# Performance work log

Measured on AMD Instinct MI355X. Metric: run time of the kernel, lower is better.

Reference implementation:

```python
import jax, jax.numpy as jnp
import numpy as np

DN = ('NCH', 'OIH', 'NCH')  # conv dimension numbers: [batch, channel, length]

def setup_inputs() -> dict:
    key = jax.random.key(0)
    ks = jax.random.split(key, 8)
    B, S, L, D, F, V = 16, 64, 128, 512, 256, 30000
    return {
        'text': jax.random.randint(ks[0], (B, S, L), 0, V),
        'embed': jax.random.normal(ks[1], (V, D), dtype=jnp.float32),
        'w3': jax.random.normal(ks[2], (F, D, 3), dtype=jnp.float32) * 0.05,
        'b3': jax.random.normal(ks[3], (F,), dtype=jnp.float32) * 0.05,
        'w4': jax.random.normal(ks[4], (F, D, 4), dtype=jnp.float32) * 0.05,
        'b4': jax.random.normal(ks[5], (F,), dtype=jnp.float32) * 0.05,
        'w5': jax.random.normal(ks[6], (F, D, 5), dtype=jnp.float32) * 0.05,
        'b5': jax.random.normal(ks[7], (F,), dtype=jnp.float32) * 0.05,
    }

def reference(text, embed, w3, b3, w4, b4, w5, b5):
    B, S, L = text.shape
    # Embed tokens, flatten episodes x utterances into one batch, channels-first.
    x = embed[text]                                   # [B, S, L, D]
    x = x.reshape(B * S, L, -1).transpose(0, 2, 1)    # [BS, D, L]
    outs = []
    for w, b in ((w3, b3), (w4, b4), (w5, b5)):
        y = jax.lax.conv_general_dilated(x, w, (1,), 'VALID', dimension_numbers=DN)
        # max-over-time pooling (valid conv -> length L-K+1)
        outs.append(jnp.max(y + b[None, :, None], axis=2))  # [BS, F]
    out = jax.nn.relu(jnp.concatenate(outs, axis=1))  # [BS, 3F]
    return out.reshape(B, S, -1)
```

## Files before the change

### kernel.cpp

```cpp
#include <hip/hip_runtime.h>
#include <hip/hip_bf16.h>


typedef __bf16 bf16x8 __attribute__((ext_vector_type(8)));
typedef float f32x16 __attribute__((ext_vector_type(16)));
typedef float f32x4v __attribute__((ext_vector_type(4)));

#define ROWS 132
#define ROWB 512
#define BUF_BYTES (ROWS * ROWB)
#define RED_OFF (2 * BUF_BYTES)
#define LDS_TOTAL (RED_OFF + 2048)

__global__ void pack_w_kernel(const float* __restrict__ w3,
                              const float* __restrict__ w4,
                              const float* __restrict__ w5,
                              __bf16* __restrict__ wq) {
    const int t    = blockIdx.x * 256 + threadIdx.x;
    const int g    = t >> 6;
    const int lane = t & 63;
    int rel, Kw; const float* w;
    if (g < 768)       { rel = g;        Kw = 3; w = w3; }
    else if (g < 1792) { rel = g - 768;  Kw = 4; w = w4; }
    else               { rel = g - 1792; Kw = 5; w = w5; }
    const int k16 = rel >> 3;
    const int n32 = rel & 7;
    const int f   = n32 * 32 + (lane & 31);
    const int tap = k16 >> 5;
    const int d0  = (k16 & 31) * 16 + (lane >> 5) * 8;
    const float* src = w + ((size_t)f * 512 + d0) * Kw + tap;
    bf16x8 o;
#pragma unroll
    for (int j = 0; j < 8; ++j) o[j] = (__bf16)src[j * Kw];
    *(bf16x8*)(wq + (size_t)t * 8) = o;
}

__global__ __launch_bounds__(1024, 4) void conv_gemm_kernel(
        const int* __restrict__ text,
        const float* __restrict__ embed,
        const __bf16* __restrict__ wq,
        const float* __restrict__ b3,
        const float* __restrict__ b4,
        const float* __restrict__ b5,
        float* __restrict__ out) {
    extern __shared__ char lds[];
    float* const red = (float*)(lds + RED_OFF);

    const int tid  = threadIdx.x;
    const int lane = tid & 63;
    const int wave = tid >> 6;
    const int wm   = wave & 1;
    const int wn   = wave >> 1;
    const int l31  = lane & 31;
    const int lh   = lane >> 5;
    const int sr   = tid >> 5;
    const int sc   = tid & 31;

    const int bsbase = blockIdx.x * 4;

    const int arow = wm * 64 + l31;
    const int tx0  = lh ^ (arow & 31);
    const int A00  = arow * 512;

    const __bf16* const bpL = wq + (size_t)wn * 512 + (size_t)lane * 8;

    f32x4v G[4];
    auto issuePair = [&](int nbs, int h, int p0) {
#pragma unroll
        for (int p = 0; p < 2; ++p) {
            const int r = (p0 + p) * 32 + sr;
            const int tok = text[nbs * 128 + r];
            const f32x4v* src = (const f32x4v*)
                (embed + (size_t)tok * 512 + h * 256 + sc * 8);
            G[p * 2]     = __builtin_nontemporal_load(src);
            G[p * 2 + 1] = __builtin_nontemporal_load(src + 1);
        }
    };
    auto writePair = [&](char* bufp, int p0) {
#pragma unroll
        for (int p = 0; p < 2; ++p) {
            const int r = (p0 + p) * 32 + sr;
            const f32x4v v0 = G[p * 2], v1 = G[p * 2 + 1];
            bf16x8 o;
            o[0] = (__bf16)v0.x; o[1] = (__bf16)v0.y;
            o[2] = (__bf16)v0.z; o[3] = (__bf16)v0.w;
            o[4] = (__bf16)v1.x; o[5] = (__bf16)v1.y;
            o[6] = (__bf16)v1.z; o[7] = (__bf16)v1.w;
            *(bf16x8*)(bufp + r * ROWB + ((sc ^ (r & 31)) << 4)) = o;
        }
    };

    f32x16 acc[2];
    bf16x8 Br[4];
    bf16x8 A[4][2];

    issuePair(bsbase, 0, 0); writePair(lds, 0);
    issuePair(bsbase, 0, 2); writePair(lds, 2);
    issuePair(bsbase, 1, 0); writePair(lds + BUF_BYTES, 0);
    issuePair(bsbase, 1, 2); writePair(lds + BUF_BYTES, 2);
    if (tid < 128) {
        const int r = 128 + sr;
        const int off = r * ROWB + ((sc ^ (r & 31)) << 4);
        bf16x8 z = {};
        *(bf16x8*)(lds + off) = z;
        *(bf16x8*)(lds + BUF_BYTES + off) = z;
    }
#pragma unroll
    for (int k = 0; k < 4; ++k)
        Br[k] = *(const bf16x8*)(bpL + (size_t)k * 4096);
    __syncthreads();

#pragma unroll 1
    for (int i = 0; i < 4; ++i) {
        const int bs  = bsbase + i;
        const int nbs = bs + 1;
        const bool stg = (i < 3);
#pragma unroll 1
        for (int c = 0; c < 3; ++c) {
            const int KW = 3 + c;
            const size_t cb  = (c == 0) ? 0 : (c == 1) ? 393216 : 917504;
            const size_t cbn = (c == 0) ? 393216 : (c == 1) ? 917504 : 0;
            const __bf16* bpc = bpL + cb;
            const __bf16* bpn = bpL + cbn;
            const bool lastc = stg && (c == 2);

#pragma unroll
            for (int r = 0; r < 16; ++r) { acc[0][r] = 0.f; acc[1][r] = 0.f; }

            if (lastc) issuePair(nbs, 0, 0);

            A[0][0] = *(const bf16x8*)(lds + A00 + (tx0 << 4));
            A[0][1] = *(const bf16x8*)(lds + A00 + (tx0 << 4) + 16384);
            A[1][0] = *(const bf16x8*)(lds + A00 + ((2 ^ tx0) << 4));
            A[1][1] = *(const bf16x8*)(lds + A00 + ((2 ^ tx0) << 4) + 16384);

#pragma unroll 1
            for (int tap = 0; tap < KW; ++tap) {
                const int row = arow + tap;
                const int tx  = lh ^ (row & 31);
                const int rb  = row * 512;
                const bool last = (tap == KW - 1);
                const int r2  = row + 1;
                const int tx2 = lh ^ (r2 & 31);
                const int rb2 = r2 * 512;
#pragma unroll
                for (int dh = 0; dh < 2; ++dh) {
                    const int bo = dh ? BUF_BYTES : 0;
                    const int s0 = tap * 32 + dh * 16;
                    const __bf16* q0 = bpc + (size_t)(s0 + 4) * 4096;
                    const __bf16* q1 = (dh == 1 && tap == KW - 1)
                                           ? bpn : (q0 + 12 * 4096);
#pragma unroll
                    for (int d = 0; d < 16; ++d) {
                        const int s = dh * 16 + d;
                        const int u = s + 2;
                        int na;
                        if (u < 16)
                            na = rb + (((2 * u) ^ tx) << 4);
                        else if (u < 32)
                            na = BUF_BYTES + rb + (((2 * (u - 16)) ^ tx) << 4);
                        else if (!last)
                            na = rb2 + (((2 * (u - 32)) ^ tx2) << 4);
                        else
                            na = rb + (tx << 4);
                        const int cs = s & 3, ps = u & 3;
                        __builtin_amdgcn_s_setprio(1);
                        acc[0] = __builtin_amdgcn_mfma_f32_32x32x16_bf16(
                            A[cs][0], Br[cs], acc[0], 0, 0, 0);
                        acc[1] = __builtin_amdgcn_mfma_f32_32x32x16_bf16(
                            A[cs][1], Br[cs], acc[1], 0, 0, 0);
                        __builtin_amdgcn_s_setprio(0);
                        A[ps][0] = *(const bf16x8*)(lds + na);
                        A[ps][1] = *(const bf16x8*)(lds + na + 16384);
                        Br[cs] = (d < 12)
                            ? *(const bf16x8*)(q0 + (size_t)d * 4096)
                            : *(const bf16x8*)(q1 + (size_t)(d - 12) * 4096);
                    }
                }
            }

            const int Tv = 126 - c;
            float cmax = -3.0e38f;
#pragma unroll
            for (int mt = 0; mt < 2; ++mt)
#pragma unroll
                for (int r = 0; r < 16; ++r) {
                    const int t = wm * 64 + mt * 32
                                + (r & 3) + 8 * (r >> 2) + 4 * lh;
                    if (t < Tv) cmax = fmaxf(cmax, acc[mt][r]);
                }
            cmax = fmaxf(cmax, __shfl_xor(cmax, 32, 64));

            __syncthreads();
            if (lane < 32) red[wm * 256 + wn * 32 + l31] = cmax;
            if (lastc) {
                writePair(lds, 0);
                issuePair(nbs, 0, 2); writePair(lds, 2);
                issuePair(nbs, 1, 0); writePair(lds + BUF_BYTES, 0);
                issuePair(nbs, 1, 2); writePair(lds + BUF_BYTES, 2);
            }
            __syncthreads();
            if (tid < 256) {
                const float* bias = (c == 0) ? b3 : (c == 1) ? b4 : b5;
                const float vv = fmaxf(red[tid], red[256 + tid]) + bias[tid];
                __builtin_nontemporal_store(fmaxf(vv, 0.f),
                    &out[(size_t)bs * 768 + c * 256 + tid]);
            }
        }
    }
}

extern "C" void kernel_launch(void* const* d_in, const int* in_sizes, int n_in,
                              void* d_out, int out_size, void* d_ws, size_t ws_size,
                              hipStream_t stream) {
    const int*   text  = (const int*)d_in[0];
    const float* embed = (const float*)d_in[1];
    const float* w3    = (const float*)d_in[2];
    const float* b3    = (const float*)d_in[3];
    const float* w4    = (const float*)d_in[4];
    const float* b4    = (const float*)d_in[5];
    const float* w5    = (const float*)d_in[6];
    const float* b5    = (const float*)d_in[7];
    float* out = (float*)d_out;

    __bf16* wq = (__bf16*)d_ws;

    (void)hipFuncSetAttribute((const void*)conv_gemm_kernel,
                              hipFuncAttributeMaxDynamicSharedMemorySize,
                              LDS_TOTAL);

    pack_w_kernel<<<768, 256, 0, stream>>>(w3, w4, w5, wq);
    conv_gemm_kernel<<<256, 1024, LDS_TOTAL, stream>>>(text, embed, wq,
                                                       b3, b4, b5, out);
}
```

Before: 493.9 us.

## Halve block to 512 threads with 2x2 MFMA tiles per wave

Reduces the conv GEMM block from 16 to 8 waves, so each wave now computes two N-tiles (64 filters) instead of one. A-fragments read from LDS are reused across two B fragments, which halves LDS A traffic per MFMA and doubles accumulator registers. Embedding staging is reworked to 16 rows per pass with four row-groups. Fewer waves per CU cut latency hiding, and register pressure rises from the larger accumulators and B buffers.

```diff
diff --git a/kernel.cpp b/kernel.cpp
--- a/kernel.cpp
+++ b/kernel.cpp
@@ -35,7 +35,7 @@
     *(bf16x8*)(wq + (size_t)t * 8) = o;
 }
 
-__global__ __launch_bounds__(1024, 4) void conv_gemm_kernel(
+__global__ __launch_bounds__(512, 2) void conv_gemm_kernel(
         const int* __restrict__ text,
         const float* __restrict__ embed,
         const __bf16* __restrict__ wq,
@@ -62,13 +62,13 @@
     const int tx0  = lh ^ (arow & 31);
     const int A00  = arow * 512;
 
-    const __bf16* const bpL = wq + (size_t)wn * 512 + (size_t)lane * 8;
-
-    f32x4v G[4];
-    auto issuePair = [&](int nbs, int h, int p0) {
-#pragma unroll
-        for (int p = 0; p < 2; ++p) {
-            const int r = (p0 + p) * 32 + sr;
+    const __bf16* const bpL = wq + (size_t)wn * 1024 + (size_t)lane * 8;
+
+    f32x4v G[8];
+    auto issueQuad = [&](int nbs, int h, int p0) {
+#pragma unroll
+        for (int p = 0; p < 4; ++p) {
+            const int r = (p0 + p) * 16 + sr;
             const int tok = text[nbs * 128 + r];
             const f32x4v* src = (const f32x4v*)
                 (embed + (size_t)tok * 512 + h * 256 + sc * 8);
@@ -76,10 +76,10 @@
             G[p * 2 + 1] = __builtin_nontemporal_load(src + 1);
         }
     };
-    auto writePair = [&](char* bufp, int p0) {
-#pragma unroll
-        for (int p = 0; p < 2; ++p) {
-            const int r = (p0 + p) * 32 + sr;
+    auto writeQuad = [&](char* bufp, int p0) {
+#pragma unroll
+        for (int p = 0; p < 4; ++p) {
+            const int r = (p0 + p) * 16 + sr;
             const f32x4v v0 = G[p * 2], v1 = G[p * 2 + 1];
             bf16x8 o;
             o[0] = (__bf16)v0.x; o[1] = (__bf16)v0.y;
@@ -90,16 +90,21 @@
         }
     };
 
-    f32x16 acc[2];
-    bf16x8 Br[4];
+    f32x16 acc[2][2];
+    bf16x8 Br[4][2];
     bf16x8 A[4][2];
 
-    issuePair(bsbase, 0, 0); writePair(lds, 0);
-    issuePair(bsbase, 0, 2); writePair(lds, 2);
-    issuePair(bsbase, 1, 0); writePair(lds + BUF_BYTES, 0);
-    issuePair(bsbase, 1, 2); writePair(lds + BUF_BYTES, 2);
+    auto loadB = [&](int slot, const __bf16* p) {
+        Br[slot][0] = *(const bf16x8*)(p);
+        Br[slot][1] = *(const bf16x8*)(p + 512);
+    };
+
+    issueQuad(bsbase, 0, 0); writeQuad(lds, 0);
+    issueQuad(bsbase, 0, 4); writeQuad(lds, 4);
+    issueQuad(bsbase, 1, 0); writeQuad(lds + BUF_BYTES, 0);
+    issueQuad(bsbase, 1, 4); writeQuad(lds + BUF_BYTES, 4);
     if (tid < 128) {
-        const int r = 128 + sr;
+        const int r = 128 + (tid >> 5);
         const int off = r * ROWB + ((sc ^ (r & 31)) << 4);
         bf16x8 z = {};
         *(bf16x8*)(lds + off) = z;
@@ -107,7 +112,7 @@
     }
 #pragma unroll
     for (int k = 0; k < 4; ++k)
-        Br[k] = *(const bf16x8*)(bpL + (size_t)k * 4096);
+        loadB(k, bpL + (size_t)k * 4096);
     __syncthreads();
 
 #pragma unroll 1
@@ -125,9 +130,13 @@
             const bool lastc = stg && (c == 2);
 
 #pragma unroll
-            for (int r = 0; r < 16; ++r) { acc[0][r] = 0.f; acc[1][r] = 0.f; }
-
-            if (lastc) issuePair(nbs, 0, 0);
+            for (int mt = 0; mt < 2; ++mt)
+#pragma unroll
+                for (int nt = 0; nt < 2; ++nt)
+#pragma unroll
+                    for (int r = 0; r < 16; ++r) acc[mt][nt][r] = 0.f;
+
+            if (lastc) issueQuad(nbs, 0, 0);
 
             A[0][0] = *(const bf16x8*)(lds + A00 + (tx0 << 4));
             A[0][1] = *(const bf16x8*)(lds + A00 + (tx0 << 4) + 16384);
@@ -145,14 +154,13 @@
                 const int rb2 = r2 * 512;
 #pragma unroll
                 for (int dh = 0; dh < 2; ++dh) {
-                    const int bo = dh ? BUF_BYTES : 0;
                     const int s0 = tap * 32 + dh * 16;
                     const __bf16* q0 = bpc + (size_t)(s0 + 4) * 4096;
-                    const __bf16* q1 = (dh == 1 && tap == KW - 1)
+                    const __bf16* q1 = (dh == 1 && last)
                                            ? bpn : (q0 + 12 * 4096);
 #pragma unroll
-                    for (int d = 0; d < 16; ++d) {
-                        const int s = dh * 16 + d;
+                    for (int j = 0; j < 16; ++j) {
+                        const int s = dh * 16 + j;
                         const int u = s + 2;
                         int na;
                         if (u < 16)
@@ -165,39 +173,51 @@
                             na = rb + (tx << 4);
                         const int cs = s & 3, ps = u & 3;
                         __builtin_amdgcn_s_setprio(1);
-                        acc[0] = __builtin_amdgcn_mfma_f32_32x32x16_bf16(
-                            A[cs][0], Br[cs], acc[0], 0, 0, 0);
-                        acc[1] = __builtin_amdgcn_mfma_f32_32x32x16_bf16(
-                            A[cs][1], Br[cs], acc[1], 0, 0, 0);
+                        acc[0][0] = __builtin_amdgcn_mfma_f32_32x32x16_bf16(
+                            A[cs][0], Br[cs][0], acc[0][0], 0, 0, 0);
+                        acc[0][1] = __builtin_amdgcn_mfma_f32_32x32x16_bf16(
+                            A[cs][0], Br[cs][1], acc[0][1], 0, 0, 0);
+                        acc[1][0] = __builtin_amdgcn_mfma_f32_32x32x16_bf16(
+                            A[cs][1], Br[cs][0], acc[1][0], 0, 0, 0);
+                        acc[1][1] = __builtin_amdgcn_mfma_f32_32x32x16_bf16(
+                            A[cs][1], Br[cs][1], acc[1][1], 0, 0, 0);
                         __builtin_amdgcn_s_setprio(0);
                         A[ps][0] = *(const bf16x8*)(lds + na);
                         A[ps][1] = *(const bf16x8*)(lds + na + 16384);
-                        Br[cs] = (d < 12)
-                            ? *(const bf16x8*)(q0 + (size_t)d * 4096)
-                            : *(const bf16x8*)(q1 + (size_t)(d - 12) * 4096);
+                        loadB(cs, (j < 12) ? (q0 + (size_t)j * 4096)
+                                           : (q1 + (size_t)(j - 12) * 4096));
                     }
                 }
             }
 
             const int Tv = 126 - c;
-            float cmax = -3.0e38f;
-#pragma unroll
-            for (int mt = 0; mt < 2; ++mt)
-#pragma unroll
-                for (int r = 0; r < 16; ++r) {
-                    const int t = wm * 64 + mt * 32
-                                + (r & 3) + 8 * (r >> 2) + 4 * lh;
-                    if (t < Tv) cmax = fmaxf(cmax, acc[mt][r]);
-                }
-            cmax = fmaxf(cmax, __shfl_xor(cmax, 32, 64));
+            float cmax[2];
+#pragma unroll
+            for (int nt = 0; nt < 2; ++nt) {
+                float mx = -3.0e38f;
+#pragma unroll
+                for (int mt = 0; mt < 2; ++mt)
+#pragma unroll
+                    for (int r = 0; r < 16; ++r) {
+                        const int t = wm * 64 + mt * 32
+                                    + (r & 3) + 8 * (r >> 2) + 4 * lh;
+                        if (t < Tv) mx = fmaxf(mx, acc[mt][nt][r]);
+                    }
+                mx = fmaxf(mx, __shfl_xor(mx, 32, 64));
+                cmax[nt] = mx;
+            }
 
             __syncthreads();
-            if (lane < 32) red[wm * 256 + wn * 32 + l31] = cmax;
+            if (lane < 32) {
+#pragma unroll
+                for (int nt = 0; nt < 2; ++nt)
+                    red[wm * 256 + wn * 64 + nt * 32 + l31] = cmax[nt];
+            }
             if (lastc) {
-                writePair(lds, 0);
-                issuePair(nbs, 0, 2); writePair(lds, 2);
-                issuePair(nbs, 1, 0); writePair(lds + BUF_BYTES, 0);
-                issuePair(nbs, 1, 2); writePair(lds + BUF_BYTES, 2);
+                writeQuad(lds, 0);
+                issueQuad(nbs, 0, 4); writeQuad(lds, 4);
+                issueQuad(nbs, 1, 0); writeQuad(lds + BUF_BYTES, 0);
+                issueQuad(nbs, 1, 4); writeQuad(lds + BUF_BYTES, 4);
             }
             __syncthreads();
             if (tid < 256) {
@@ -230,6 +250,6 @@
                               LDS_TOTAL);
 
     pack_w_kernel<<<768, 256, 0, stream>>>(w3, w4, w5, wq);
-    conv_gemm_kernel<<<256, 1024, LDS_TOTAL, stream>>>(text, embed, wq,
-                                                       b3, b4, b5, out);
+    conv_gemm_kernel<<<256, 512, LDS_TOTAL, stream>>>(text, embed, wq,
+                                                      b3, b4, b5, out);
 }
```

New measurement: 458.6 us. -7.2%, faster.
